# Kernel tuning notes

Measured on AMD Instinct MI355X. Metric: run time of the kernel, lower is better.

The kernel has to match this reference:

```python
import jax, jax.numpy as jnp
import numpy as np

T, B, H = 256, 64, 1024


def _lstm_layer(x, w_ih, w_hh, b_ih, b_hh):
    # x: (T, B, H); w_ih, w_hh: (4H, H); biases: (4H,)
    # Precompute input-to-gate GEMM for all timesteps (compute-bound part).
    xg = jnp.einsum('tbh,gh->tbg', x, w_ih) + (b_ih + b_hh)  # (T, B, 4H)

    def step(carry, xg_t):
        h, c = carry
        gates = xg_t + h @ w_hh.T  # (B, 4H)
        i, f, g, o = jnp.split(gates, 4, axis=-1)  # PyTorch gate order i,f,g,o
        i = jax.nn.sigmoid(i)
        f = jax.nn.sigmoid(f)
        g = jnp.tanh(g)
        o = jax.nn.sigmoid(o)
        c = f * c + i * g
        h = o * jnp.tanh(c)
        return (h, c), h

    h0 = jnp.zeros((x.shape[1], w_hh.shape[1]), x.dtype)
    (_, _), hs = jax.lax.scan(step, (h0, h0), xg)
    return hs  # (T, B, H)


def setup_inputs() -> dict:
    key = jax.random.key(0)
    ks = jax.random.split(key, 9)
    u = lambda k, shape: jax.random.uniform(k, shape, jnp.float32, -0.1, 0.1)
    return {
        'x': jax.random.normal(ks[0], (T, B, H), jnp.float32),
        'w_ih5': u(ks[1], (4 * H, H)),
        'w_hh5': u(ks[2], (4 * H, H)),
        'b_ih5': u(ks[3], (4 * H,)),
        'b_hh5': u(ks[4], (4 * H,)),
        'w_ih6': u(ks[5], (4 * H, H)),
        'w_hh6': u(ks[6], (4 * H, H)),
        'b_ih6': u(ks[7], (4 * H,)),
        'b_hh6': u(ks[8], (4 * H,)),
    }


def reference(x, w_ih5, w_hh5, b_ih5, b_hh5, w_ih6, w_hh6, b_ih6, b_hh6):
    out5 = _lstm_layer(x, w_ih5, w_hh5, b_ih5, b_hh5) + x
    out6 = _lstm_layer(out5, w_ih6, w_hh6, b_ih6, b_hh6) + out5
    return out6
```

## Files before the change

### kernel.cpp

```cpp
#include <hip/hip_runtime.h>


#define TT 256
#define BB 64
#define HH 1024
#define GG 128
#define BH (BB * HH)

typedef __attribute__((ext_vector_type(8))) short short8;
typedef __attribute__((ext_vector_type(4))) float float4v;
typedef __attribute__((ext_vector_type(2))) float float2v;

__device__ __forceinline__ unsigned short f2bf(float f) {
  unsigned u = __builtin_bit_cast(unsigned, f);
  u += 0x7fffu + ((u >> 16) & 1u);
  return (unsigned short)(u >> 16);
}
__device__ __forceinline__ float bf2f(unsigned short s) {
  unsigned u = ((unsigned)s) << 16;
  return __builtin_bit_cast(float, u);
}
__device__ __forceinline__ float fexp2(float x) { return __builtin_amdgcn_exp2f(x); }
__device__ __forceinline__ float frcp(float x) { return __builtin_amdgcn_rcpf(x); }
__device__ __forceinline__ float sigm(float x) {
  return frcp(1.0f + fexp2(-1.4426950408889634f * x));
}
__device__ __forceinline__ float tanha(float x) {
  return 1.0f - 2.0f * frcp(1.0f + fexp2(2.8853900817779268f * x));
}

__global__ __launch_bounds__(256) void cvt_x_blocked(const float* __restrict__ in,
                                                     unsigned short* __restrict__ out) {
  const int i = blockIdx.x * 256 + threadIdx.x;
  const int t = i >> 13;
  const int r = i & 8191;
  const int c = r >> 6;
  const int b = r & 63;
  const float* src = in + ((size_t)t << 16) + b * 1024 + (c << 3);
  const float4v a = *(const float4v*)src;
  const float4v d = *(const float4v*)(src + 4);
  short8 v;
  v[0] = (short)f2bf(a[0]); v[1] = (short)f2bf(a[1]);
  v[2] = (short)f2bf(a[2]); v[3] = (short)f2bf(a[3]);
  v[4] = (short)f2bf(d[0]); v[5] = (short)f2bf(d[1]);
  v[6] = (short)f2bf(d[2]); v[7] = (short)f2bf(d[3]);
  *(short8*)(out + ((size_t)t << 16) + c * 512 + b * 8) = v;
}

__global__ __launch_bounds__(256, 1) void lstm2_fused(
    const float* __restrict__ x,
    const float* __restrict__ wih5, const float* __restrict__ whh5,
    const float* __restrict__ bih5, const float* __restrict__ bhh5,
    const float* __restrict__ wih6, const float* __restrict__ whh6,
    const float* __restrict__ bih6, const float* __restrict__ bhh6,
    unsigned short* __restrict__ buf, unsigned short* __restrict__ hbuf5,
    unsigned short* __restrict__ hbuf6, float* __restrict__ out,
    int* __restrict__ flags5, int* __restrict__ flagsO,
    int* __restrict__ flags6) {
  const int xcd = (int)(blockIdx.x & 7);
  const int role = (xcd >= 4) ? 1 : 0;
  const int p = (int)(blockIdx.x >> 3) * 4 + (xcd & 3);
  const int tid = threadIdx.x;
  const int w = tid >> 6;
  const int lane = tid & 63;
  const int ln = lane & 15;
  const int q = lane >> 4;

  __shared__ float gp[4][BB][35];

  const float* wih = role ? wih6 : wih5;
  const float* whh = role ? whh6 : whh5;
  const float* bih = role ? bih6 : bih5;
  const float* bhh = role ? bhh6 : bhh5;
  unsigned short* hbuf = role ? hbuf6 : hbuf5;
  int* hflags = role ? flags6 : flags5;

  short8 wfx[16], wfh[16];
#pragma unroll
  for (int kk = 0; kk < 8; ++kk) {
#pragma unroll
    for (int nt = 0; nt < 2; ++nt) {
      const int n = 16 * nt + ln;
      const int gidx = (n >> 3) * HH + p * 8 + (n & 7);
      const int k0 = 256 * w + kk * 32 + 8 * q;
      const float* sx = wih + (size_t)gidx * HH + k0;
      const float* sh = whh + (size_t)gidx * HH + k0;
      short8 vx, vh;
#pragma unroll
      for (int j = 0; j < 8; ++j) { vx[j] = (short)f2bf(sx[j]); vh[j] = (short)f2bf(sh[j]); }
      wfx[kk * 2 + nt] = vx;
      wfh[kk * 2 + nt] = vh;
    }
  }

  const int eb = lane;
  const int jj0 = w;
  float bsum[2][4];
#pragma unroll
  for (int s = 0; s < 2; ++s) {
    const int jj = 2 * jj0 + s;
#pragma unroll
    for (int gt = 0; gt < 4; ++gt) {
      const int gidx = gt * HH + p * 8 + jj;
      bsum[s][gt] = bih[gidx] + bhh[gidx];
    }
  }
  float cst[2] = {0.f, 0.f};
  unsigned po_prev = 0;

  size_t rh[4];
#pragma unroll
  for (int mt = 0; mt < 4; ++mt)
    rh[mt] = (size_t)(16 * mt + ln) * 8 + (size_t)(256 * w + 8 * q) * 64;

  for (int t = 0; t < TT; ++t) {
    float4v acc[4][2];
#pragma unroll
    for (int mt = 0; mt < 4; ++mt)
#pragma unroll
      for (int nt = 0; nt < 2; ++nt)
        acc[mt][nt] = (float4v){0.f, 0.f, 0.f, 0.f};

    if (role == 0) {
      const unsigned short* Ab = buf + (size_t)t * BH;
#pragma unroll
      for (int kk = 0; kk < 8; ++kk) {
        short8 af[4];
#pragma unroll
        for (int mt = 0; mt < 4; ++mt)
          af[mt] = *(const short8*)(Ab + rh[mt] + (size_t)kk * 2048);
#pragma unroll
        for (int mt = 0; mt < 4; ++mt) {
          acc[mt][0] = __builtin_amdgcn_mfma_f32_16x16x32_bf16(af[mt], wfx[kk * 2 + 0], acc[mt][0], 0, 0, 0);
          acc[mt][1] = __builtin_amdgcn_mfma_f32_16x16x32_bf16(af[mt], wfx[kk * 2 + 1], acc[mt][1], 0, 0, 0);
        }
      }
      if (t > 0) {
        if (w == 0) {
          int* fl = flags5 + (size_t)(t - 1) * GG;
          for (;;) {
            const int a0 = __hip_atomic_load(fl + lane, __ATOMIC_RELAXED, __HIP_MEMORY_SCOPE_AGENT);
            const int a1 = __hip_atomic_load(fl + 64 + lane, __ATOMIC_RELAXED, __HIP_MEMORY_SCOPE_AGENT);
            if (__all((a0 != 0) & (a1 != 0))) break;
            __builtin_amdgcn_s_sleep(2);
          }
        }
        __builtin_amdgcn_fence(__ATOMIC_ACQUIRE, "workgroup");
        __syncthreads();
      }
    } else {
      if (w == 0) {
        int* fo = flagsO + (size_t)t * GG;
        int* fh = flags6 + (size_t)(t > 0 ? t - 1 : 0) * GG;
        for (;;) {
          const int a0 = __hip_atomic_load(fo + lane, __ATOMIC_RELAXED, __HIP_MEMORY_SCOPE_AGENT);
          const int a1 = __hip_atomic_load(fo + 64 + lane, __ATOMIC_RELAXED, __HIP_MEMORY_SCOPE_AGENT);
          int ok = (a0 != 0) & (a1 != 0);
          if (t > 0) {
            const int b0 = __hip_atomic_load(fh + lane, __ATOMIC_RELAXED, __HIP_MEMORY_SCOPE_AGENT);
            const int b1 = __hip_atomic_load(fh + 64 + lane, __ATOMIC_RELAXED, __HIP_MEMORY_SCOPE_AGENT);
            ok &= (b0 != 0) & (b1 != 0);
          }
          if (__all(ok)) break;
          __builtin_amdgcn_s_sleep(2);
        }
      }
      __builtin_amdgcn_fence(__ATOMIC_ACQUIRE, "workgroup");
      __syncthreads();
      const unsigned short* Ab = buf + (size_t)t * BH;
#pragma unroll
      for (int kk = 0; kk < 8; ++kk) {
        short8 af[4];
#pragma unroll
        for (int mt = 0; mt < 4; ++mt)
          af[mt] = *(const short8*)(Ab + rh[mt] + (size_t)kk * 2048);
#pragma unroll
        for (int mt = 0; mt < 4; ++mt) {
          acc[mt][0] = __builtin_amdgcn_mfma_f32_16x16x32_bf16(af[mt], wfx[kk * 2 + 0], acc[mt][0], 0, 0, 0);
          acc[mt][1] = __builtin_amdgcn_mfma_f32_16x16x32_bf16(af[mt], wfx[kk * 2 + 1], acc[mt][1], 0, 0, 0);
        }
      }
    }

    if (t > 0) {
      const unsigned short* Hb = hbuf + (size_t)(t - 1) * BH;
#pragma unroll
      for (int kk = 0; kk < 8; ++kk) {
        short8 af[4];
#pragma unroll
        for (int mt = 0; mt < 4; ++mt)
          af[mt] = *(const short8*)(Hb + rh[mt] + (size_t)kk * 2048);
#pragma unroll
        for (int mt = 0; mt < 4; ++mt) {
          acc[mt][0] = __builtin_amdgcn_mfma_f32_16x16x32_bf16(af[mt], wfh[kk * 2 + 0], acc[mt][0], 0, 0, 0);
          acc[mt][1] = __builtin_amdgcn_mfma_f32_16x16x32_bf16(af[mt], wfh[kk * 2 + 1], acc[mt][1], 0, 0, 0);
        }
      }
    }

#pragma unroll
    for (int mt = 0; mt < 4; ++mt)
#pragma unroll
      for (int nt = 0; nt < 2; ++nt)
#pragma unroll
        for (int r = 0; r < 4; ++r)
          gp[w][16 * mt + 4 * q + r][16 * nt + ln] = acc[mt][nt][r];

    __syncthreads();

    const size_t tb = (size_t)t * BH;
    const size_t hidx = tb + (size_t)p * 512 + (size_t)eb * 8 + 2 * jj0;
    float hv[2];
#pragma unroll
    for (int s = 0; s < 2; ++s) {
      const int jj = 2 * jj0 + s;
      float iv = bsum[s][0], fv = bsum[s][1], gv = bsum[s][2], ov = bsum[s][3];
#pragma unroll
      for (int ww = 0; ww < 4; ++ww) {
        iv += gp[ww][eb][jj];
        fv += gp[ww][eb][8 + jj];
        gv += gp[ww][eb][16 + jj];
        ov += gp[ww][eb][24 + jj];
      }
      const float ig = sigm(iv);
      const float fg = sigm(fv);
      const float gg_ = tanha(gv);
      const float og = sigm(ov);
      const float c = fg * cst[s] + ig * gg_;
      cst[s] = c;
      hv[s] = og * tanha(c);
    }
    {
      unsigned packed = (unsigned)f2bf(hv[0]) | ((unsigned)f2bf(hv[1]) << 16);
      __hip_atomic_store((unsigned*)(hbuf + hidx), packed, __ATOMIC_RELAXED,
                         __HIP_MEMORY_SCOPE_AGENT);
    }
    asm volatile("s_waitcnt vmcnt(0)" ::: "memory");
    __syncthreads();
    if (tid == 0)
      __hip_atomic_store(hflags + (size_t)t * GG + p, 1, __ATOMIC_RELAXED,
                         __HIP_MEMORY_SCOPE_AGENT);

    if (role == 0) {
      if (t > 0) {
        __hip_atomic_store((unsigned*)(buf + (hidx - BH)), po_prev, __ATOMIC_RELAXED,
                           __HIP_MEMORY_SCOPE_AGENT);
        asm volatile("s_waitcnt vmcnt(0)" ::: "memory");
        __syncthreads();
        if (tid == 0)
          __hip_atomic_store(flagsO + (size_t)(t - 1) * GG + p, 1, __ATOMIC_RELAXED,
                             __HIP_MEMORY_SCOPE_AGENT);
      }
      const float2v r = *(const float2v*)(x + tb + (size_t)eb * HH + p * 8 + 2 * jj0);
      const float o0 = hv[0] + r[0];
      const float o1 = hv[1] + r[1];
      po_prev = (unsigned)f2bf(o0) | ((unsigned)f2bf(o1) << 16);
    } else {
      const unsigned rb = *(const unsigned*)(buf + hidx);
      const float o0 = hv[0] + bf2f((unsigned short)(rb & 0xffff));
      const float o1 = hv[1] + bf2f((unsigned short)(rb >> 16));
      float2v vo; vo[0] = o0; vo[1] = o1;
      *(float2v*)(out + tb + (size_t)eb * HH + p * 8 + 2 * jj0) = vo;
    }
  }

  if (role == 0) {
    if (w == 0) {
      int* fl = flags5 + (size_t)(TT - 1) * GG;
      for (;;) {
        const int a0 = __hip_atomic_load(fl + lane, __ATOMIC_RELAXED, __HIP_MEMORY_SCOPE_AGENT);
        const int a1 = __hip_atomic_load(fl + 64 + lane, __ATOMIC_RELAXED, __HIP_MEMORY_SCOPE_AGENT);
        if (__all((a0 != 0) & (a1 != 0))) break;
        __builtin_amdgcn_s_sleep(2);
      }
    }
    __builtin_amdgcn_fence(__ATOMIC_ACQUIRE, "workgroup");
    __syncthreads();
    const size_t hlast = (size_t)(TT - 1) * BH + (size_t)p * 512 + (size_t)eb * 8 + 2 * jj0;
    __hip_atomic_store((unsigned*)(buf + hlast), po_prev, __ATOMIC_RELAXED,
                       __HIP_MEMORY_SCOPE_AGENT);
    asm volatile("s_waitcnt vmcnt(0)" ::: "memory");
    __syncthreads();
    if (tid == 0)
      __hip_atomic_store(flagsO + (size_t)(TT - 1) * GG + p, 1, __ATOMIC_RELAXED,
                         __HIP_MEMORY_SCOPE_AGENT);
  }
}

extern "C" void kernel_launch(void* const* d_in, const int* in_sizes, int n_in,
                              void* d_out, int out_size, void* d_ws, size_t ws_size,
                              hipStream_t stream) {
  const float* x    = (const float*)d_in[0];
  const float* wih5 = (const float*)d_in[1];
  const float* whh5 = (const float*)d_in[2];
  const float* bih5 = (const float*)d_in[3];
  const float* bhh5 = (const float*)d_in[4];
  const float* wih6 = (const float*)d_in[5];
  const float* whh6 = (const float*)d_in[6];
  const float* bih6 = (const float*)d_in[7];
  const float* bhh6 = (const float*)d_in[8];
  float* out = (float*)d_out;

  char* ws = (char*)d_ws;
  unsigned short* buf   = (unsigned short*)(ws);
  unsigned short* hbuf5 = (unsigned short*)(ws + 33554432);
  unsigned short* hbuf6 = (unsigned short*)(ws + 67108864);
  int* flags            = (int*)(ws + 100663296);
  int* flags5 = flags;
  int* flagsO = flags + TT * GG;
  int* flags6 = flags + 2 * TT * GG;

  hipMemsetAsync(flags, 0, 3 * TT * GG * sizeof(int), stream);

  cvt_x_blocked<<<dim3(TT * BB * HH / 8 / 256), dim3(256), 0, stream>>>(x, buf);

  lstm2_fused<<<dim3(2 * GG), dim3(256), 0, stream>>>(
      x, wih5, whh5, bih5, bhh5, wih6, whh6, bih6, bhh6,
      buf, hbuf5, hbuf6, out, flags5, flagsO, flags6);
}
```

Baseline: 2.836 ms.

## Halve persistent block count, each block owning 16 hidden units per layer

New measurement: 5.380 ms. +89.7%, slower.

```diff
diff --git a/kernel.cpp b/kernel.cpp
--- a/kernel.cpp
+++ b/kernel.cpp
@@ -4,7 +4,7 @@
 #define TT 256
 #define BB 64
 #define HH 1024
-#define GG 128
+#define CB 64
 #define BH (BB * HH)
 
 typedef __attribute__((ext_vector_type(8))) short short8;
@@ -66,7 +66,7 @@
   const int ln = lane & 15;
   const int q = lane >> 4;
 
-  __shared__ float gp[4][BB][35];
+  __shared__ float gp[4][BB][67];
 
   const float* wih = role ? wih6 : wih5;
   const float* whh = role ? whh6 : whh5;
@@ -75,50 +75,50 @@
   unsigned short* hbuf = role ? hbuf6 : hbuf5;
   int* hflags = role ? flags6 : flags5;
 
-  short8 wfx[16], wfh[16];
+  short8 wfx[32], wfh[32];
 #pragma unroll
   for (int kk = 0; kk < 8; ++kk) {
 #pragma unroll
-    for (int nt = 0; nt < 2; ++nt) {
-      const int n = 16 * nt + ln;
-      const int gidx = (n >> 3) * HH + p * 8 + (n & 7);
+    for (int nt = 0; nt < 4; ++nt) {
+      const int gidx = nt * HH + p * 16 + ln;
       const int k0 = 256 * w + kk * 32 + 8 * q;
       const float* sx = wih + (size_t)gidx * HH + k0;
       const float* sh = whh + (size_t)gidx * HH + k0;
       short8 vx, vh;
 #pragma unroll
       for (int j = 0; j < 8; ++j) { vx[j] = (short)f2bf(sx[j]); vh[j] = (short)f2bf(sh[j]); }
-      wfx[kk * 2 + nt] = vx;
-      wfh[kk * 2 + nt] = vh;
+      wfx[kk * 4 + nt] = vx;
+      wfh[kk * 4 + nt] = vh;
     }
   }
 
   const int eb = lane;
-  const int jj0 = w;
-  float bsum[2][4];
-#pragma unroll
-  for (int s = 0; s < 2; ++s) {
-    const int jj = 2 * jj0 + s;
+  float bsum[4][4];
+#pragma unroll
+  for (int s = 0; s < 4; ++s) {
+    const int jj = 4 * w + s;
 #pragma unroll
     for (int gt = 0; gt < 4; ++gt) {
-      const int gidx = gt * HH + p * 8 + jj;
+      const int gidx = gt * HH + p * 16 + jj;
       bsum[s][gt] = bih[gidx] + bhh[gidx];
     }
   }
-  float cst[2] = {0.f, 0.f};
-  unsigned po_prev = 0;
+  float cst[4] = {0.f, 0.f, 0.f, 0.f};
+  unsigned po_prev0 = 0, po_prev1 = 0;
 
   size_t rh[4];
 #pragma unroll
   for (int mt = 0; mt < 4; ++mt)
     rh[mt] = (size_t)(16 * mt + ln) * 8 + (size_t)(256 * w + 8 * q) * 64;
 
+  const size_t hoff = (size_t)(p * 2 + (w >> 1)) * 512 + (size_t)eb * 8 + 4 * (w & 1);
+
   for (int t = 0; t < TT; ++t) {
-    float4v acc[4][2];
+    float4v acc[4][4];
 #pragma unroll
     for (int mt = 0; mt < 4; ++mt)
 #pragma unroll
-      for (int nt = 0; nt < 2; ++nt)
+      for (int nt = 0; nt < 4; ++nt)
         acc[mt][nt] = (float4v){0.f, 0.f, 0.f, 0.f};
 
     if (role == 0) {
@@ -130,18 +130,17 @@
         for (int mt = 0; mt < 4; ++mt)
           af[mt] = *(const short8*)(Ab + rh[mt] + (size_t)kk * 2048);
 #pragma unroll
-        for (int mt = 0; mt < 4; ++mt) {
-          acc[mt][0] = __builtin_amdgcn_mfma_f32_16x16x32_bf16(af[mt], wfx[kk * 2 + 0], acc[mt][0], 0, 0, 0);
-          acc[mt][1] = __builtin_amdgcn_mfma_f32_16x16x32_bf16(af[mt], wfx[kk * 2 + 1], acc[mt][1], 0, 0, 0);
-        }
+        for (int mt = 0; mt < 4; ++mt)
+#pragma unroll
+          for (int nt = 0; nt < 4; ++nt)
+            acc[mt][nt] = __builtin_amdgcn_mfma_f32_16x16x32_bf16(af[mt], wfx[kk * 4 + nt], acc[mt][nt], 0, 0, 0);
       }
       if (t > 0) {
         if (w == 0) {
-          int* fl = flags5 + (size_t)(t - 1) * GG;
+          int* fl = flags5 + (size_t)(t - 1) * CB;
           for (;;) {
             const int a0 = __hip_atomic_load(fl + lane, __ATOMIC_RELAXED, __HIP_MEMORY_SCOPE_AGENT);
-            const int a1 = __hip_atomic_load(fl + 64 + lane, __ATOMIC_RELAXED, __HIP_MEMORY_SCOPE_AGENT);
-            if (__all((a0 != 0) & (a1 != 0))) break;
+            if (__all(a0 != 0)) break;
             __builtin_amdgcn_s_sleep(2);
           }
         }
@@ -150,16 +149,14 @@
       }
     } else {
       if (w == 0) {
-        int* fo = flagsO + (size_t)t * GG;
-        int* fh = flags6 + (size_t)(t > 0 ? t - 1 : 0) * GG;
+        int* fo = flagsO + (size_t)t * CB;
+        int* fh = flags6 + (size_t)(t > 0 ? t - 1 : 0) * CB;
         for (;;) {
           const int a0 = __hip_atomic_load(fo + lane, __ATOMIC_RELAXED, __HIP_MEMORY_SCOPE_AGENT);
-          const int a1 = __hip_atomic_load(fo + 64 + lane, __ATOMIC_RELAXED, __HIP_MEMORY_SCOPE_AGENT);
-          int ok = (a0 != 0) & (a1 != 0);
+          int ok = (a0 != 0);
           if (t > 0) {
             const int b0 = __hip_atomic_load(fh + lane, __ATOMIC_RELAXED, __HIP_MEMORY_SCOPE_AGENT);
-            const int b1 = __hip_atomic_load(fh + 64 + lane, __ATOMIC_RELAXED, __HIP_MEMORY_SCOPE_AGENT);
-            ok &= (b0 != 0) & (b1 != 0);
+            ok &= (b0 != 0);
           }
           if (__all(ok)) break;
           __builtin_amdgcn_s_sleep(2);
@@ -175,10 +172,10 @@
         for (int mt = 0; mt < 4; ++mt)
           af[mt] = *(const short8*)(Ab + rh[mt] + (size_t)kk * 2048);
 #pragma unroll
-        for (int mt = 0; mt < 4; ++mt) {
-          acc[mt][0] = __builtin_amdgcn_mfma_f32_16x16x32_bf16(af[mt], wfx[kk * 2 + 0], acc[mt][0], 0, 0, 0);
-          acc[mt][1] = __builtin_amdgcn_mfma_f32_16x16x32_bf16(af[mt], wfx[kk * 2 + 1], acc[mt][1], 0, 0, 0);
-        }
+        for (int mt = 0; mt < 4; ++mt)
+#pragma unroll
+          for (int nt = 0; nt < 4; ++nt)
+            acc[mt][nt] = __builtin_amdgcn_mfma_f32_16x16x32_bf16(af[mt], wfx[kk * 4 + nt], acc[mt][nt], 0, 0, 0);
       }
     }
 
@@ -191,17 +188,17 @@
         for (int mt = 0; mt < 4; ++mt)
           af[mt] = *(const short8*)(Hb + rh[mt] + (size_t)kk * 2048);
 #pragma unroll
-        for (int mt = 0; mt < 4; ++mt) {
-          acc[mt][0] = __builtin_amdgcn_mfma_f32_16x16x32_bf16(af[mt], wfh[kk * 2 + 0], acc[mt][0], 0, 0, 0);
-          acc[mt][1] = __builtin_amdgcn_mfma_f32_16x16x32_bf16(af[mt], wfh[kk * 2 + 1], acc[mt][1], 0, 0, 0);
-        }
+        for (int mt = 0; mt < 4; ++mt)
+#pragma unroll
+          for (int nt = 0; nt < 4; ++nt)
+            acc[mt][nt] = __builtin_amdgcn_mfma_f32_16x16x32_bf16(af[mt], wfh[kk * 4 + nt], acc[mt][nt], 0, 0, 0);
       }
     }
 
 #pragma unroll
     for (int mt = 0; mt < 4; ++mt)
 #pragma unroll
-      for (int nt = 0; nt < 2; ++nt)
+      for (int nt = 0; nt < 4; ++nt)
 #pragma unroll
         for (int r = 0; r < 4; ++r)
           gp[w][16 * mt + 4 * q + r][16 * nt + ln] = acc[mt][nt][r];
@@ -209,18 +206,18 @@
     __syncthreads();
 
     const size_t tb = (size_t)t * BH;
-    const size_t hidx = tb + (size_t)p * 512 + (size_t)eb * 8 + 2 * jj0;
-    float hv[2];
-#pragma unroll
-    for (int s = 0; s < 2; ++s) {
-      const int jj = 2 * jj0 + s;
+    const size_t hidx = tb + hoff;
+    float hv[4];
+#pragma unroll
+    for (int s = 0; s < 4; ++s) {
+      const int jj = 4 * w + s;
       float iv = bsum[s][0], fv = bsum[s][1], gv = bsum[s][2], ov = bsum[s][3];
 #pragma unroll
       for (int ww = 0; ww < 4; ++ww) {
         iv += gp[ww][eb][jj];
-        fv += gp[ww][eb][8 + jj];
-        gv += gp[ww][eb][16 + jj];
-        ov += gp[ww][eb][24 + jj];
+        fv += gp[ww][eb][16 + jj];
+        gv += gp[ww][eb][32 + jj];
+        ov += gp[ww][eb][48 + jj];
       }
       const float ig = sigm(iv);
       const float fg = sigm(fv);
@@ -231,58 +228,66 @@
       hv[s] = og * tanha(c);
     }
     {
-      unsigned packed = (unsigned)f2bf(hv[0]) | ((unsigned)f2bf(hv[1]) << 16);
-      __hip_atomic_store((unsigned*)(hbuf + hidx), packed, __ATOMIC_RELAXED,
+      const unsigned u0 = (unsigned)f2bf(hv[0]) | ((unsigned)f2bf(hv[1]) << 16);
+      const unsigned u1 = (unsigned)f2bf(hv[2]) | ((unsigned)f2bf(hv[3]) << 16);
+      __hip_atomic_store((unsigned*)(hbuf + hidx), u0, __ATOMIC_RELAXED,
+                         __HIP_MEMORY_SCOPE_AGENT);
+      __hip_atomic_store((unsigned*)(hbuf + hidx + 2), u1, __ATOMIC_RELAXED,
                          __HIP_MEMORY_SCOPE_AGENT);
     }
     asm volatile("s_waitcnt vmcnt(0)" ::: "memory");
     __syncthreads();
     if (tid == 0)
-      __hip_atomic_store(hflags + (size_t)t * GG + p, 1, __ATOMIC_RELAXED,
+      __hip_atomic_store(hflags + (size_t)t * CB + p, 1, __ATOMIC_RELAXED,
                          __HIP_MEMORY_SCOPE_AGENT);
 
     if (role == 0) {
       if (t > 0) {
-        __hip_atomic_store((unsigned*)(buf + (hidx - BH)), po_prev, __ATOMIC_RELAXED,
+        __hip_atomic_store((unsigned*)(buf + (hidx - BH)), po_prev0, __ATOMIC_RELAXED,
+                           __HIP_MEMORY_SCOPE_AGENT);
+        __hip_atomic_store((unsigned*)(buf + (hidx - BH) + 2), po_prev1, __ATOMIC_RELAXED,
                            __HIP_MEMORY_SCOPE_AGENT);
         asm volatile("s_waitcnt vmcnt(0)" ::: "memory");
         __syncthreads();
         if (tid == 0)
-          __hip_atomic_store(flagsO + (size_t)(t - 1) * GG + p, 1, __ATOMIC_RELAXED,
+          __hip_atomic_store(flagsO + (size_t)(t - 1) * CB + p, 1, __ATOMIC_RELAXED,
                              __HIP_MEMORY_SCOPE_AGENT);
       }
-      const float2v r = *(const float2v*)(x + tb + (size_t)eb * HH + p * 8 + 2 * jj0);
-      const float o0 = hv[0] + r[0];
-      const float o1 = hv[1] + r[1];
-      po_prev = (unsigned)f2bf(o0) | ((unsigned)f2bf(o1) << 16);
+      const float4v r = *(const float4v*)(x + tb + (size_t)eb * HH + p * 16 + 4 * w);
+      po_prev0 = (unsigned)f2bf(hv[0] + r[0]) | ((unsigned)f2bf(hv[1] + r[1]) << 16);
+      po_prev1 = (unsigned)f2bf(hv[2] + r[2]) | ((unsigned)f2bf(hv[3] + r[3]) << 16);
     } else {
-      const unsigned rb = *(const unsigned*)(buf + hidx);
-      const float o0 = hv[0] + bf2f((unsigned short)(rb & 0xffff));
-      const float o1 = hv[1] + bf2f((unsigned short)(rb >> 16));
-      float2v vo; vo[0] = o0; vo[1] = o1;
-      *(float2v*)(out + tb + (size_t)eb * HH + p * 8 + 2 * jj0) = vo;
+      const unsigned rb0 = *(const unsigned*)(buf + hidx);
+      const unsigned rb1 = *(const unsigned*)(buf + hidx + 2);
+      float4v vo;
+      vo[0] = hv[0] + bf2f((unsigned short)(rb0 & 0xffff));
+      vo[1] = hv[1] + bf2f((unsigned short)(rb0 >> 16));
+      vo[2] = hv[2] + bf2f((unsigned short)(rb1 & 0xffff));
+      vo[3] = hv[3] + bf2f((unsigned short)(rb1 >> 16));
+      *(float4v*)(out + tb + (size_t)eb * HH + p * 16 + 4 * w) = vo;
     }
   }
 
   if (role == 0) {
     if (w == 0) {
-      int* fl = flags5 + (size_t)(TT - 1) * GG;
+      int* fl = flags5 + (size_t)(TT - 1) * CB;
       for (;;) {
         const int a0 = __hip_atomic_load(fl + lane, __ATOMIC_RELAXED, __HIP_MEMORY_SCOPE_AGENT);
-        const int a1 = __hip_atomic_load(fl + 64 + lane, __ATOMIC_RELAXED, __HIP_MEMORY_SCOPE_AGENT);
-        if (__all((a0 != 0) & (a1 != 0))) break;
+        if (__all(a0 != 0)) break;
         __builtin_amdgcn_s_sleep(2);
       }
     }
     __builtin_amdgcn_fence(__ATOMIC_ACQUIRE, "workgroup");
     __syncthreads();
-    const size_t hlast = (size_t)(TT - 1) * BH + (size_t)p * 512 + (size_t)eb * 8 + 2 * jj0;
-    __hip_atomic_store((unsigned*)(buf + hlast), po_prev, __ATOMIC_RELAXED,
+    const size_t hlast = (size_t)(TT - 1) * BH + hoff;
+    __hip_atomic_store((unsigned*)(buf + hlast), po_prev0, __ATOMIC_RELAXED,
+                       __HIP_MEMORY_SCOPE_AGENT);
+    __hip_atomic_store((unsigned*)(buf + hlast + 2), po_prev1, __ATOMIC_RELAXED,
                        __HIP_MEMORY_SCOPE_AGENT);
     asm volatile("s_waitcnt vmcnt(0)" ::: "memory");
     __syncthreads();
     if (tid == 0)
-      __hip_atomic_store(flagsO + (size_t)(TT - 1) * GG + p, 1, __ATOMIC_RELAXED,
+      __hip_atomic_store(flagsO + (size_t)(TT - 1) * CB + p, 1, __ATOMIC_RELAXED,
                          __HIP_MEMORY_SCOPE_AGENT);
   }
 }
@@ -307,14 +312,14 @@
   unsigned short* hbuf6 = (unsigned short*)(ws + 67108864);
   int* flags            = (int*)(ws + 100663296);
   int* flags5 = flags;
-  int* flagsO = flags + TT * GG;
-  int* flags6 = flags + 2 * TT * GG;
-
-  hipMemsetAsync(flags, 0, 3 * TT * GG * sizeof(int), stream);
+  int* flagsO = flags + TT * CB;
+  int* flags6 = flags + 2 * TT * CB;
+
+  hipMemsetAsync(flags, 0, 3 * TT * CB * sizeof(int), stream);
 
   cvt_x_blocked<<<dim3(TT * BB * HH / 8 / 256), dim3(256), 0, stream>>>(x, buf);
 
-  lstm2_fused<<<dim3(2 * GG), dim3(256), 0, stream>>>(
+  lstm2_fused<<<dim3(2 * CB), dim3(256), 0, stream>>>(
       x, wih5, whh5, bih5, bhh5, wih6, whh6, bih6, bhh6,
       buf, hbuf5, hbuf6, out, flags5, flagsO, flags6);
 }
```
